# Performance work log

Hardware: AMD Instinct MI355X
Metric: run time of the kernel (lower is better)

## Reference

```python
import jax, jax.numpy as jnp
import numpy as np
import math
from jax import lax

B, L = 64, 8192
S = L // 8          # width after 3 stride-(1,2) SAME convs
D = 4 * 5           # height(4) * channels(5) -> per-token feature dim
D_FLAT = S * D


def setup_inputs():
    key = jax.random.key(0)
    ks = jax.random.split(key, 32)
    sc = 0.1
    inp = {
        "inputs": jax.random.randint(ks[0], (B, L), 0, 4, dtype=jnp.int32),
        # conv stack: HWIO kernels, Conv2D(5,(4,4),(1,2),'SAME')
        "conv_w1": sc * jax.random.normal(ks[1], (4, 4, 1, 5), jnp.float32),
        "conv_b1": jnp.zeros((5,), jnp.float32),
        "conv_w2": sc * jax.random.normal(ks[2], (4, 4, 5, 5), jnp.float32),
        "conv_b2": jnp.zeros((5,), jnp.float32),
        "conv_w3": sc * jax.random.normal(ks[3], (4, 4, 5, 5), jnp.float32),
        "conv_b3": jnp.zeros((5,), jnp.float32),
        # 3 SelfAttn blocks, each with K/Q/V projections [D, D]
        "attn1_K": sc * jax.random.normal(ks[4], (D, D), jnp.float32),
        "attn1_Q": sc * jax.random.normal(ks[5], (D, D), jnp.float32),
        "attn1_V": sc * jax.random.normal(ks[6], (D, D), jnp.float32),
        "attn2_K": sc * jax.random.normal(ks[7], (D, D), jnp.float32),
        "attn2_Q": sc * jax.random.normal(ks[8], (D, D), jnp.float32),
        "attn2_V": sc * jax.random.normal(ks[9], (D, D), jnp.float32),
        "attn3_K": sc * jax.random.normal(ks[10], (D, D), jnp.float32),
        "attn3_Q": sc * jax.random.normal(ks[11], (D, D), jnp.float32),
        "attn3_V": sc * jax.random.normal(ks[12], (D, D), jnp.float32),
        # 3 Dense(10) layers (no activation, as in Keras defaults)
        "dense_w1": 0.01 * jax.random.normal(ks[13], (D_FLAT, 10), jnp.float32),
        "dense_b1": jnp.zeros((10,), jnp.float32),
        "dense_w2": sc * jax.random.normal(ks[14], (10, 10), jnp.float32),
        "dense_b2": jnp.zeros((10,), jnp.float32),
        "dense_w3": sc * jax.random.normal(ks[15], (10, 10), jnp.float32),
        "dense_b3": jnp.zeros((10,), jnp.float32),
    }
    return inp


def _conv(x, w, b):
    # NHWC, HWIO, strides (1,2), SAME
    y = lax.conv_general_dilated(x, w, window_strides=(1, 2), padding="SAME",
                                 dimension_numbers=("NHWC", "HWIO", "NHWC"))
    return y + b


def _self_attn(x, Kw, Qw, Vw):
    # x: [B, S, D]; manual causal scaled dot-product attention
    K = x @ Kw
    Q = x @ Qw
    V = x @ Vw
    s = Q.shape[1]
    mask = jnp.triu(jnp.full((s, s), -jnp.inf, dtype=x.dtype), k=1)
    scores = jnp.einsum("bsd,btd->bst", Q, K) / math.sqrt(K.shape[-1]) + mask
    return jax.nn.softmax(scores, axis=-1) @ V


def reference(inputs, conv_w1, conv_b1, conv_w2, conv_b2, conv_w3, conv_b3,
              attn1_K, attn1_Q, attn1_V, attn2_K, attn2_Q, attn2_V,
              attn3_K, attn3_Q, attn3_V,
              dense_w1, dense_b1, dense_w2, dense_b2, dense_w3, dense_b3):
    # one_hot over axis=1 -> [B, 4, L], then channel dim -> [B, 4, L, 1]
    x = jax.nn.one_hot(inputs, 4, axis=1, dtype=jnp.float32)[..., None]
    x = _conv(x, conv_w1, conv_b1)
    x = _conv(x, conv_w2, conv_b2)
    x = _conv(x, conv_w3, conv_b3)            # [B, 4, S, 5]
    # tokens along width, features = height(4) x channels(5)
    x = jnp.transpose(x, (0, 2, 1, 3)).reshape(x.shape[0], S, D)
    x = _self_attn(x, attn1_K, attn1_Q, attn1_V)
    x = _self_attn(x, attn2_K, attn2_Q, attn2_V)
    x = _self_attn(x, attn3_K, attn3_Q, attn3_V)
    x = x.reshape(x.shape[0], -1)             # flatten [B, S*D]
    x = x @ dense_w1 + dense_b1
    x = x @ dense_w2 + dense_b2
    x = x @ dense_w3 + dense_b3               # [B, 10]
    return x
```

## Files before the change

### kernel.cpp

```cpp
#include <hip/hip_runtime.h>
#include <hip/hip_bf16.h>


#define B_ 64
#define L_ 8192
#define S_ 1024
#define D_ 20

typedef unsigned short ushort_t;
typedef __attribute__((ext_vector_type(8))) short short8_t;
typedef __attribute__((ext_vector_type(4))) short short4_t;
typedef __attribute__((ext_vector_type(4))) float f32x4_t;

__device__ __forceinline__ ushort_t f2bf(float f) {
  unsigned u = __float_as_uint(f);
  return (ushort_t)((u + 0x7fffu + ((u >> 16) & 1u)) >> 16);
}
__device__ __forceinline__ float bf2f(ushort_t h) {
  return __uint_as_float(((unsigned)h) << 16);
}

__global__ __launch_bounds__(256) void conv12_kernel(
    const int* __restrict__ inp,
    const float* __restrict__ W1c, const float* __restrict__ B1c,
    const float* __restrict__ W2c, const float* __restrict__ B2c,
    float* __restrict__ out,
    const float* __restrict__ W1d,
    float* __restrict__ W1T) {
  __shared__ float w1s[80], b1s[5], w2s[400], b2s[5];
  for (int j = threadIdx.x; j < 400; j += 256) w2s[j] = W2c[j];
  if (threadIdx.x < 80)      w1s[threadIdx.x]      = W1c[threadIdx.x];
  else if (threadIdx.x < 85) b1s[threadIdx.x - 80] = B1c[threadIdx.x - 80];
  else if (threadIdx.x < 90) b2s[threadIdx.x - 85] = B2c[threadIdx.x - 85];
  __syncthreads();
  const int idx = blockIdx.x * 256 + threadIdx.x;
  const int b  = idx >> 11;
  const int wo = idx & 2047;
  const int* ib = inp + (size_t)b * L_;
  int iv[10];
#pragma unroll
  for (int t = 0; t < 10; ++t) {
    int g = 4 * wo - 3 + t;
    iv[t] = (g >= 0 && g < L_) ? ib[g] : -100;
  }
  float val[4][4][5];
#pragma unroll
  for (int pos = 0; pos < 4; ++pos) {
    const int w1 = 2 * wo - 1 + pos;
    const bool okp = (w1 >= 0 && w1 < 4096);
#pragma unroll
    for (int hi = 0; hi < 4; ++hi)
#pragma unroll
      for (int ci = 0; ci < 5; ++ci) val[hi][pos][ci] = okp ? b1s[ci] : 0.f;
    if (okp) {
#pragma unroll
      for (int kw = 0; kw < 4; ++kw) {
        const int gw = 2 * w1 - 1 + kw;
        if (gw >= 0 && gw < L_) {
          const int v = iv[2 * pos + kw];
#pragma unroll
          for (int hi = 0; hi < 4; ++hi) {
            const int kh = v - hi + 1;
            if (kh >= 0 && kh < 4) {
#pragma unroll
              for (int ci = 0; ci < 5; ++ci)
                val[hi][pos][ci] += w1s[(kh * 4 + kw) * 5 + ci];
            }
          }
        }
      }
    }
  }
  float acc[4][5];
#pragma unroll
  for (int h = 0; h < 4; ++h)
#pragma unroll
    for (int c = 0; c < 5; ++c) acc[h][c] = b2s[c];
#pragma unroll
  for (int kh = 0; kh < 4; ++kh)
#pragma unroll
    for (int kw = 0; kw < 4; ++kw)
#pragma unroll
      for (int ci = 0; ci < 5; ++ci) {
        const float* wp = w2s + ((kh * 4 + kw) * 5 + ci) * 5;
        float w0 = wp[0], w1v = wp[1], w2v = wp[2], w3 = wp[3], w4 = wp[4];
#pragma unroll
        for (int h = 0; h < 4; ++h) {
          int hi = h - 1 + kh;
          if (hi >= 0 && hi < 4) {
            float x = val[hi][kw][ci];
            acc[h][0] += w0 * x;  acc[h][1] += w1v * x; acc[h][2] += w2v * x;
            acc[h][3] += w3 * x;  acc[h][4] += w4 * x;
          }
        }
      }
  float* ob = out + (size_t)b * 4 * 2048 * 5;
#pragma unroll
  for (int h = 0; h < 4; ++h)
#pragma unroll
    for (int c = 0; c < 5; ++c) ob[(h * 2048 + wo) * 5 + c] = acc[h][c];
  for (int j = idx; j < 204800; j += 131072) {
    int col = j / 20480, i2 = j - col * 20480;
    W1T[j] = W1d[i2 * 10 + col];
  }
}

__global__ __launch_bounds__(256) void conv3_proj_kernel(
    const float* __restrict__ in,
    const float* __restrict__ W,  const float* __restrict__ Bi,
    const float* __restrict__ Kw, const float* __restrict__ Qw,
    const float* __restrict__ Vw,
    ushort_t* __restrict__ Qb, ushort_t* __restrict__ Kb,
    ushort_t* __restrict__ Vt) {
  constexpr int WIN = 2048;
  __shared__ float ws[400], bs[5];
  __shared__ float kw[400], qw[400], vw[400];
  for (int j = threadIdx.x; j < 400; j += 256) {
    ws[j] = W[j]; kw[j] = Kw[j]; qw[j] = Qw[j]; vw[j] = Vw[j];
  }
  if (threadIdx.x < 5) bs[threadIdx.x] = Bi[threadIdx.x];
  __syncthreads();
  const int r  = blockIdx.x * 256 + threadIdx.x;
  const int b  = r >> 10;
  const int wo = r & 1023;
  float val[4][4][5];
#pragma unroll
  for (int hi = 0; hi < 4; ++hi) {
    const float* ir = in + ((size_t)b * 4 + hi) * WIN * 5;
#pragma unroll
    for (int kwp = 0; kwp < 4; ++kwp) {
      int wi = 2 * wo - 1 + kwp;
      bool ok = (wi >= 0 && wi < WIN);
#pragma unroll
      for (int ci = 0; ci < 5; ++ci) val[hi][kwp][ci] = ok ? ir[wi * 5 + ci] : 0.f;
    }
  }
  float acc[4][5];
#pragma unroll
  for (int h = 0; h < 4; ++h)
#pragma unroll
    for (int c = 0; c < 5; ++c) acc[h][c] = bs[c];
#pragma unroll
  for (int kh = 0; kh < 4; ++kh)
#pragma unroll
    for (int kwp = 0; kwp < 4; ++kwp)
#pragma unroll
      for (int ci = 0; ci < 5; ++ci) {
        const float* wp = ws + ((kh * 4 + kwp) * 5 + ci) * 5;
        float w0 = wp[0], w1 = wp[1], w2 = wp[2], w3 = wp[3], w4 = wp[4];
#pragma unroll
        for (int h = 0; h < 4; ++h) {
          int hi = h - 1 + kh;
          if (hi >= 0 && hi < 4) {
            float x = val[hi][kwp][ci];
            acc[h][0] += w0 * x; acc[h][1] += w1 * x; acc[h][2] += w2 * x;
            acc[h][3] += w3 * x; acc[h][4] += w4 * x;
          }
        }
      }
  float x[D_];
#pragma unroll
  for (int h = 0; h < 4; ++h)
#pragma unroll
    for (int c = 0; c < 5; ++c) x[h * 5 + c] = acc[h][c];
  float q[D_], k[D_], v[D_];
#pragma unroll
  for (int j = 0; j < D_; ++j) { q[j] = 0.f; k[j] = 0.f; v[j] = 0.f; }
#pragma unroll
  for (int i = 0; i < D_; ++i) {
#pragma unroll
    for (int j = 0; j < D_; ++j) {
      q[j] += x[i] * qw[i * D_ + j];
      k[j] += x[i] * kw[i * D_ + j];
      v[j] += x[i] * vw[i * D_ + j];
    }
  }
  const float sc = 0.22360679774997896f;
  ushort_t qt[32], kt[32];
#pragma unroll
  for (int j = 0; j < D_; ++j) { qt[j] = f2bf(q[j] * sc); kt[j] = f2bf(k[j]); }
#pragma unroll
  for (int j = D_; j < 32; ++j) { qt[j] = 0; kt[j] = 0; }
  int4* qd = (int4*)(Qb + (size_t)r * 32);
  int4* kd = (int4*)(Kb + (size_t)r * 32);
#pragma unroll
  for (int j = 0; j < 4; ++j) {
    qd[j] = *(const int4*)(qt + 8 * j);
    kd[j] = *(const int4*)(kt + 8 * j);
  }
  ushort_t* vbase = Vt + ((size_t)b * 32) * 1024 + wo;
#pragma unroll
  for (int d = 0; d < D_; ++d) vbase[d * 1024] = f2bf(v[d]);
}

#define TT_ 128
template <bool FUSE>
__global__ __launch_bounds__(256) void attn_kernel(
    const ushort_t* __restrict__ Qb, const ushort_t* __restrict__ Kb,
    const ushort_t* __restrict__ Vt,
    const float* __restrict__ Kw2, const float* __restrict__ Qw2,
    const float* __restrict__ Vw2,
    ushort_t* __restrict__ Qb2, ushort_t* __restrict__ Kb2,
    ushort_t* __restrict__ Vt2,
    const float* __restrict__ W1T,
    float* __restrict__ part2) {
  const int b     = blockIdx.y;
  const int g     = (blockIdx.y >> 4) & 3;
  const int off   = 4 * (g >> 1);
  const int strip = (g & 1) ? ((15 - off - blockIdx.x) & 15)
                            : (((int)blockIdx.x + off) & 15);
  const int q0    = strip * 64;
  const int tid   = threadIdx.x;
  const int w     = tid >> 6;
  const int lane  = tid & 63;
  const int n     = lane & 15;
  const int quad  = lane >> 4;
  const int qbase = q0 + 16 * w;
  const int qg    = qbase + n;
  __shared__ ushort_t kts[128 * 40];
  __shared__ ushort_t vts[32 * 136];
  __shared__ float extraf[FUSE ? 2480 : 3840];
  if (FUSE) {
    float tmp[5];
#pragma unroll
    for (int u = 0; u < 5; ++u) {
      int j = tid + u * 256;
      if (j < 1200) {
        int m = j / 400, oo = j - m * 400;
        tmp[u] = (m == 0) ? Kw2[oo] : (m == 1) ? Qw2[oo] : Vw2[oo];
      }
    }
#pragma unroll
    for (int u = 0; u < 5; ++u) {
      int j = tid + u * 256;
      if (j < 1200) extraf[j] = tmp[u];
    }
  }
  const ushort_t* KbB = Kb + (size_t)b * 1024 * 32;
  const ushort_t* VtB = Vt + (size_t)b * 32 * 1024;
  short8_t qfrag = *(const short8_t*)(Qb + ((size_t)(b * 1024 + qbase + n)) * 32 + quad * 8);
  f32x4_t oA = {0.f, 0.f, 0.f, 0.f};
  f32x4_t oB = {0.f, 0.f, 0.f, 0.f};
  float lsum = 0.f;
  const f32x4_t zero = {0.f, 0.f, 0.f, 0.f};
  const int nt = q0 + 64;
  for (int t0 = 0; t0 < nt; t0 += TT_) {
    __syncthreads();
    for (int i = tid; i < 512; i += 256) {
      int row = i >> 2, qc = i & 3;
      *(int4*)(kts + row * 40 + qc * 8) =
          *(const int4*)(KbB + (size_t)(t0 + row) * 32 + qc * 8);
    }
    for (int i = tid; i < 320; i += 256) {
      int row = i >> 4, cc = i & 15;
      *(int4*)(vts + row * 136 + cc * 8) =
          *(const int4*)(VtB + (size_t)row * 1024 + t0 + cc * 8);
    }
    __syncthreads();
    short8_t kf[8];
#pragma unroll
    for (int hc = 0; hc < 8; ++hc)
      kf[hc] = *(const short8_t*)(kts + (hc * 16 + n) * 40 + quad * 8);
#pragma unroll
    for (int hc = 0; hc < 8; ++hc) {
      const int tg = t0 + hc * 16 + quad * 4;
      f32x4_t s = __builtin_amdgcn_mfma_f32_16x16x32_bf16(kf[hc], qfrag, zero, 0, 0, 0);
      ushort_t pk4[4];
#pragma unroll
      for (int r = 0; r < 4; ++r) {
        float p = (tg + r <= qg) ? __expf(s[r]) : 0.f;
        ushort_t h = f2bf(p);
        lsum += bf2f(h);
        pk4[r] = h;
      }
      short4_t pfrag = *(const short4_t*)pk4;
      short4_t vlo = *(const short4_t*)(vts + n * 136 + hc * 16 + quad * 4);
      short4_t vhi = *(const short4_t*)(vts + (16 + n) * 136 + hc * 16 + quad * 4);
      oA = __builtin_amdgcn_mfma_f32_16x16x16bf16_1k(vlo, pfrag, oA, 0, 0, 0);
      oB = __builtin_amdgcn_mfma_f32_16x16x16bf16_1k(vhi, pfrag, oB, 0, 0, 0);
    }
  }
  float l = lsum;
  l += __shfl_xor(l, 16, 64);
  l += __shfl_xor(l, 32, 64);
  const float inv = 1.f / l;
  if (FUSE) {
    float* pw  = extraf;
    float* oxw = extraf + 1200 + w * 320;
#pragma unroll
    for (int r = 0; r < 4; ++r) oxw[n * 20 + quad * 4 + r] = oA[r] * inv;
    if (quad == 0) {
#pragma unroll
      for (int r = 0; r < 4; ++r) oxw[n * 20 + 16 + r] = oB[r] * inv;
    }
    __asm__ volatile("s_waitcnt lgkmcnt(0)" ::: "memory");
    const int row  = lane >> 2;
    const int part = lane & 3;
    float x[D_];
#pragma unroll
    for (int i = 0; i < D_; ++i) x[i] = oxw[row * 20 + i];
    float qv[5], kv[5], vv[5];
#pragma unroll
    for (int jj = 0; jj < 5; ++jj) { qv[jj] = 0.f; kv[jj] = 0.f; vv[jj] = 0.f; }
#pragma unroll
    for (int i = 0; i < D_; ++i) {
      const float xi = x[i];
#pragma unroll
      for (int jj = 0; jj < 5; ++jj) {
        const int j = 5 * part + jj;
        kv[jj] += xi * pw[i * 20 + j];
        qv[jj] += xi * pw[400 + i * 20 + j];
        vv[jj] += xi * pw[800 + i * 20 + j];
      }
    }
    const float sc = 0.22360679774997896f;
    const int rg = b * 1024 + qbase + row;
    const int s  = rg & 1023;
#pragma unroll
    for (int jj = 0; jj < 5; ++jj) {
      const int j = 5 * part + jj;
      Kb2[(size_t)rg * 32 + j] = f2bf(kv[jj]);
      Qb2[(size_t)rg * 32 + j] = f2bf(qv[jj] * sc);
      Vt2[(size_t)b * 32768 + (size_t)j * 1024 + s] = f2bf(vv[jj]);
    }
    if (part == 0) {
#pragma unroll
      for (int u = 0; u < 6; ++u)
        *(unsigned*)(Kb2 + (size_t)rg * 32 + 20 + 2 * u) = 0u;
    } else if (part == 1) {
#pragma unroll
      for (int u = 0; u < 6; ++u)
        *(unsigned*)(Qb2 + (size_t)rg * 32 + 20 + 2 * u) = 0u;
    }
  } else {
    float* oxflat = extraf;
    float* oxw    = oxflat + w * 320;
    float* red    = extraf + 1280;
#pragma unroll
    for (int r = 0; r < 4; ++r) oxw[n * 20 + quad * 4 + r] = oA[r] * inv;
    if (quad == 0) {
#pragma unroll
      for (int r = 0; r < 4; ++r) oxw[n * 20 + 16 + r] = oB[r] * inv;
    }
    __syncthreads();
    float acc[10];
#pragma unroll
    for (int j = 0; j < 10; ++j) acc[j] = 0.f;
    const float* wb = W1T;
    const int base = q0 * 20;
#pragma unroll
    for (int k = 0; k < 5; ++k) {
      const int il = tid + 256 * k;
      const float xv = oxflat[il];
#pragma unroll
      for (int j = 0; j < 10; ++j)
        acc[j] += xv * wb[(size_t)j * 20480 + base + il];
    }
#pragma unroll
    for (int j = 0; j < 10; ++j) red[tid * 10 + j] = acc[j];
    __syncthreads();
    for (int off2 = 128; off2 > 0; off2 >>= 1) {
      if (tid < off2) {
#pragma unroll
        for (int j = 0; j < 10; ++j) red[tid * 10 + j] += red[(tid + off2) * 10 + j];
      }
      __syncthreads();
    }
    if (tid < 10) part2[((b << 4) + strip) * 10 + tid] = red[tid];
  }
}

__global__ __launch_bounds__(64) void dense_final(
    const float* __restrict__ part2,
    const float* __restrict__ B1,
    const float* __restrict__ W2, const float* __restrict__ B2,
    const float* __restrict__ W3, const float* __restrict__ B3,
    float* __restrict__ out) {
  const int b = blockIdx.x;
  __shared__ float y1[10], y2[10];
  if (threadIdx.x < 10) {
    int j = threadIdx.x;
    float s = 0.f;
#pragma unroll
    for (int st = 0; st < 16; ++st) s += part2[((b << 4) + st) * 10 + j];
    y1[j] = s + B1[j];
  }
  __syncthreads();
  if (threadIdx.x < 10) {
    int j = threadIdx.x;
    float s = B2[j];
#pragma unroll
    for (int i = 0; i < 10; ++i) s += y1[i] * W2[i * 10 + j];
    y2[j] = s;
  }
  __syncthreads();
  if (threadIdx.x < 10) {
    int j = threadIdx.x;
    float s = B3[j];
#pragma unroll
    for (int i = 0; i < 10; ++i) s += y2[i] * W3[i * 10 + j];
    out[b * 10 + j] = s;
  }
}

extern "C" void kernel_launch(void* const* d_in, const int* in_sizes, int n_in,
                              void* d_out, int out_size, void* d_ws, size_t ws_size,
                              hipStream_t stream) {
  const int*   inp = (const int*)d_in[0];
  const float* cw1 = (const float*)d_in[1];
  const float* cb1 = (const float*)d_in[2];
  const float* cw2 = (const float*)d_in[3];
  const float* cb2 = (const float*)d_in[4];
  const float* cw3 = (const float*)d_in[5];
  const float* cb3 = (const float*)d_in[6];
  const float* a1K = (const float*)d_in[7];
  const float* a1Q = (const float*)d_in[8];
  const float* a1V = (const float*)d_in[9];
  const float* a2K = (const float*)d_in[10];
  const float* a2Q = (const float*)d_in[11];
  const float* a2V = (const float*)d_in[12];
  const float* a3K = (const float*)d_in[13];
  const float* a3Q = (const float*)d_in[14];
  const float* a3V = (const float*)d_in[15];
  const float* dw1 = (const float*)d_in[16];
  const float* db1 = (const float*)d_in[17];
  const float* dw2 = (const float*)d_in[18];
  const float* db2 = (const float*)d_in[19];
  const float* dw3 = (const float*)d_in[20];
  const float* db3 = (const float*)d_in[21];
  float* outp = (float*)d_out;

  float* wsf = (float*)d_ws;
  ushort_t* qbA  = (ushort_t*)(wsf);
  ushort_t* kbA  = (ushort_t*)(wsf + 1048576);
  ushort_t* vtA  = (ushort_t*)(wsf + 2097152);
  float*    part2= wsf + 4456448;
  float*    w1t  = wsf + 4466688;
  ushort_t* qbB  = (ushort_t*)(wsf + 4671488);
  ushort_t* kbB  = (ushort_t*)(wsf + 5712384);
  ushort_t* vtB  = (ushort_t*)(wsf + 6760960);
  float*    c2   = wsf + 5242880;

  conv12_kernel<<<512, 256, 0, stream>>>(inp, cw1, cb1, cw2, cb2, c2, dw1, w1t);

  conv3_proj_kernel<<<256, 256, 0, stream>>>(c2, cw3, cb3, a1K, a1Q, a1V, qbA, kbA, vtA);
  attn_kernel<true><<<dim3(16, 64), 256, 0, stream>>>(
      qbA, kbA, vtA, a2K, a2Q, a2V, qbB, kbB, vtB, nullptr, nullptr);
  attn_kernel<true><<<dim3(16, 64), 256, 0, stream>>>(
      qbB, kbB, vtB, a3K, a3Q, a3V, qbA, kbA, vtA, nullptr, nullptr);
  attn_kernel<false><<<dim3(16, 64), 256, 0, stream>>>(
      qbA, kbA, vtA, nullptr, nullptr, nullptr, nullptr, nullptr, nullptr,
      w1t, part2);

  dense_final<<<64, 64, 0, stream>>>(part2, db1, dw2, db2, dw3, db3, outp);
}
```

Baseline: 216.2 us.

## Load K/V fragments directly from global memory, dropping LDS staging in attention

The attention loop no longer stages 128-key K and V tiles in shared memory behind two barriers per iteration. Each wave now reads its MFMA fragments straight from global memory in 64-key steps and relies on L1/L2 for reuse across waves. This removes the per-tile syncthreads and LDS traffic, frees shared memory for occupancy, and drops wasted keys past the causal limit. The cost is redundant global loads by each of the four waves and less coalesced strided V reads. A barrier is added before the fused epilogue so extraf is written before it is read.

```diff
diff --git a/kernel.cpp b/kernel.cpp
--- a/kernel.cpp
+++ b/kernel.cpp
@@ -193,7 +193,6 @@
   for (int d = 0; d < D_; ++d) vbase[d * 1024] = f2bf(v[d]);
 }
 
-#define TT_ 128
 template <bool FUSE>
 __global__ __launch_bounds__(256) void attn_kernel(
     const ushort_t* __restrict__ Qb, const ushort_t* __restrict__ Kb,
@@ -217,8 +216,6 @@
   const int quad  = lane >> 4;
   const int qbase = q0 + 16 * w;
   const int qg    = qbase + n;
-  __shared__ ushort_t kts[128 * 40];
-  __shared__ ushort_t vts[32 * 136];
   __shared__ float extraf[FUSE ? 2480 : 3840];
   if (FUSE) {
     float tmp[5];
@@ -243,28 +240,21 @@
   f32x4_t oB = {0.f, 0.f, 0.f, 0.f};
   float lsum = 0.f;
   const f32x4_t zero = {0.f, 0.f, 0.f, 0.f};
-  const int nt = q0 + 64;
-  for (int t0 = 0; t0 < nt; t0 += TT_) {
-    __syncthreads();
-    for (int i = tid; i < 512; i += 256) {
-      int row = i >> 2, qc = i & 3;
-      *(int4*)(kts + row * 40 + qc * 8) =
-          *(const int4*)(KbB + (size_t)(t0 + row) * 32 + qc * 8);
-    }
-    for (int i = tid; i < 320; i += 256) {
-      int row = i >> 4, cc = i & 15;
-      *(int4*)(vts + row * 136 + cc * 8) =
-          *(const int4*)(VtB + (size_t)row * 1024 + t0 + cc * 8);
-    }
-    __syncthreads();
-    short8_t kf[8];
-#pragma unroll
-    for (int hc = 0; hc < 8; ++hc)
-      kf[hc] = *(const short8_t*)(kts + (hc * 16 + n) * 40 + quad * 8);
-#pragma unroll
-    for (int hc = 0; hc < 8; ++hc) {
-      const int tg = t0 + hc * 16 + quad * 4;
-      f32x4_t s = __builtin_amdgcn_mfma_f32_16x16x32_bf16(kf[hc], qfrag, zero, 0, 0, 0);
+  const int niter = strip + 1;
+  for (int it = 0; it < niter; ++it) {
+    const int t0 = it * 64;
+    short8_t kf[4];
+    short4_t vl[4], vh[4];
+#pragma unroll
+    for (int j = 0; j < 4; ++j) {
+      kf[j] = *(const short8_t*)(KbB + (size_t)(t0 + j * 16 + n) * 32 + quad * 8);
+      vl[j] = *(const short4_t*)(VtB + (size_t)n * 1024 + t0 + j * 16 + quad * 4);
+      vh[j] = *(const short4_t*)(VtB + (size_t)(16 + n) * 1024 + t0 + j * 16 + quad * 4);
+    }
+#pragma unroll
+    for (int j = 0; j < 4; ++j) {
+      const int tg = t0 + j * 16 + quad * 4;
+      f32x4_t s = __builtin_amdgcn_mfma_f32_16x16x32_bf16(kf[j], qfrag, zero, 0, 0, 0);
       ushort_t pk4[4];
 #pragma unroll
       for (int r = 0; r < 4; ++r) {
@@ -274,10 +264,8 @@
         pk4[r] = h;
       }
       short4_t pfrag = *(const short4_t*)pk4;
-      short4_t vlo = *(const short4_t*)(vts + n * 136 + hc * 16 + quad * 4);
-      short4_t vhi = *(const short4_t*)(vts + (16 + n) * 136 + hc * 16 + quad * 4);
-      oA = __builtin_amdgcn_mfma_f32_16x16x16bf16_1k(vlo, pfrag, oA, 0, 0, 0);
-      oB = __builtin_amdgcn_mfma_f32_16x16x16bf16_1k(vhi, pfrag, oB, 0, 0, 0);
+      oA = __builtin_amdgcn_mfma_f32_16x16x16bf16_1k(vl[j], pfrag, oA, 0, 0, 0);
+      oB = __builtin_amdgcn_mfma_f32_16x16x16bf16_1k(vh[j], pfrag, oB, 0, 0, 0);
     }
   }
   float l = lsum;
@@ -285,6 +273,7 @@
   l += __shfl_xor(l, 32, 64);
   const float inv = 1.f / l;
   if (FUSE) {
+    __syncthreads();
     float* pw  = extraf;
     float* oxw = extraf + 1200 + w * 320;
 #pragma unroll
```

After: 267.0 us. 23.5% more time.

## Split causal attention across key tiles with separate combine-and-project kernels

Applied to the files above, without the earlier changes.

Each attention layer is split key-wise, flash-decoding style. Every block handles one 128-key tile for a 64-query strip, covering only the tiles on or below the causal diagonal, and writes unnormalized partial outputs and row sums to a workspace. A combine kernel then sums the partials, normalizes, and applies the next layer's projection or the first dense layer. This evens out the causal load imbalance and greatly raises the block count, at the cost of extra kernel launches and a large fp32 partial buffer written to and read back from global memory.

```diff
diff --git a/kernel.cpp b/kernel.cpp
--- a/kernel.cpp
+++ b/kernel.cpp
@@ -193,181 +193,177 @@
   for (int d = 0; d < D_; ++d) vbase[d * 1024] = f2bf(v[d]);
 }
 
-#define TT_ 128
-template <bool FUSE>
-__global__ __launch_bounds__(256) void attn_kernel(
+__global__ __launch_bounds__(256) void attn_core(
     const ushort_t* __restrict__ Qb, const ushort_t* __restrict__ Kb,
     const ushort_t* __restrict__ Vt,
-    const float* __restrict__ Kw2, const float* __restrict__ Qw2,
-    const float* __restrict__ Vw2,
-    ushort_t* __restrict__ Qb2, ushort_t* __restrict__ Kb2,
-    ushort_t* __restrict__ Vt2,
-    const float* __restrict__ W1T,
-    float* __restrict__ part2) {
-  const int b     = blockIdx.y;
-  const int g     = (blockIdx.y >> 4) & 3;
-  const int off   = 4 * (g >> 1);
-  const int strip = (g & 1) ? ((15 - off - blockIdx.x) & 15)
-                            : (((int)blockIdx.x + off) & 15);
-  const int q0    = strip * 64;
-  const int tid   = threadIdx.x;
-  const int w     = tid >> 6;
-  const int lane  = tid & 63;
-  const int n     = lane & 15;
-  const int quad  = lane >> 4;
-  const int qbase = q0 + 16 * w;
-  const int qg    = qbase + n;
-  __shared__ ushort_t kts[128 * 40];
+    float* __restrict__ Opart,
+    float* __restrict__ lpart) {
+  const int id = blockIdx.x;
+  const int b  = id & 63;
+  int j = id >> 6;
+  int tg = 0;
+  while (j >= 16 - 2 * tg) { j -= 16 - 2 * tg; ++tg; }
+  const int sub  = j;
+  const int tid  = threadIdx.x;
+  const int w    = tid >> 6;
+  const int lane = tid & 63;
+  const int n    = lane & 15;
+  const int quad = lane >> 4;
+  const int qb   = 8 * tg + sub * 4 + w;
+  const int t0   = tg * 128;
   __shared__ ushort_t vts[32 * 136];
-  __shared__ float extraf[FUSE ? 2480 : 3840];
-  if (FUSE) {
-    float tmp[5];
-#pragma unroll
-    for (int u = 0; u < 5; ++u) {
-      int j = tid + u * 256;
-      if (j < 1200) {
-        int m = j / 400, oo = j - m * 400;
-        tmp[u] = (m == 0) ? Kw2[oo] : (m == 1) ? Qw2[oo] : Vw2[oo];
-      }
-    }
-#pragma unroll
-    for (int u = 0; u < 5; ++u) {
-      int j = tid + u * 256;
-      if (j < 1200) extraf[j] = tmp[u];
-    }
+  const ushort_t* VtB = Vt + (size_t)b * 32 * 1024;
+  for (int i = tid; i < 320; i += 256) {
+    int row = i >> 4, cc = i & 15;
+    *(int4*)(vts + row * 136 + cc * 8) =
+        *(const int4*)(VtB + (size_t)row * 1024 + t0 + cc * 8);
   }
   const ushort_t* KbB = Kb + (size_t)b * 1024 * 32;
-  const ushort_t* VtB = Vt + (size_t)b * 32 * 1024;
-  short8_t qfrag = *(const short8_t*)(Qb + ((size_t)(b * 1024 + qbase + n)) * 32 + quad * 8);
+  const int qg = qb * 16 + n;
+  short8_t qfrag = *(const short8_t*)(Qb + ((size_t)(b * 1024 + qb * 16 + n)) * 32 + quad * 8);
+  short8_t kf[8];
+#pragma unroll
+  for (int c = 0; c < 8; ++c)
+    kf[c] = *(const short8_t*)(KbB + (size_t)(t0 + c * 16 + n) * 32 + quad * 8);
   f32x4_t oA = {0.f, 0.f, 0.f, 0.f};
   f32x4_t oB = {0.f, 0.f, 0.f, 0.f};
+  const f32x4_t zero = {0.f, 0.f, 0.f, 0.f};
   float lsum = 0.f;
-  const f32x4_t zero = {0.f, 0.f, 0.f, 0.f};
-  const int nt = q0 + 64;
-  for (int t0 = 0; t0 < nt; t0 += TT_) {
-    __syncthreads();
-    for (int i = tid; i < 512; i += 256) {
-      int row = i >> 2, qc = i & 3;
-      *(int4*)(kts + row * 40 + qc * 8) =
-          *(const int4*)(KbB + (size_t)(t0 + row) * 32 + qc * 8);
-    }
-    for (int i = tid; i < 320; i += 256) {
-      int row = i >> 4, cc = i & 15;
-      *(int4*)(vts + row * 136 + cc * 8) =
-          *(const int4*)(VtB + (size_t)row * 1024 + t0 + cc * 8);
-    }
-    __syncthreads();
-    short8_t kf[8];
-#pragma unroll
-    for (int hc = 0; hc < 8; ++hc)
-      kf[hc] = *(const short8_t*)(kts + (hc * 16 + n) * 40 + quad * 8);
-#pragma unroll
-    for (int hc = 0; hc < 8; ++hc) {
-      const int tg = t0 + hc * 16 + quad * 4;
-      f32x4_t s = __builtin_amdgcn_mfma_f32_16x16x32_bf16(kf[hc], qfrag, zero, 0, 0, 0);
-      ushort_t pk4[4];
-#pragma unroll
-      for (int r = 0; r < 4; ++r) {
-        float p = (tg + r <= qg) ? __expf(s[r]) : 0.f;
-        ushort_t h = f2bf(p);
-        lsum += bf2f(h);
-        pk4[r] = h;
-      }
-      short4_t pfrag = *(const short4_t*)pk4;
-      short4_t vlo = *(const short4_t*)(vts + n * 136 + hc * 16 + quad * 4);
-      short4_t vhi = *(const short4_t*)(vts + (16 + n) * 136 + hc * 16 + quad * 4);
-      oA = __builtin_amdgcn_mfma_f32_16x16x16bf16_1k(vlo, pfrag, oA, 0, 0, 0);
-      oB = __builtin_amdgcn_mfma_f32_16x16x16bf16_1k(vhi, pfrag, oB, 0, 0, 0);
-    }
+  __syncthreads();
+#pragma unroll
+  for (int c = 0; c < 8; ++c) {
+    const int tgl = t0 + c * 16 + quad * 4;
+    f32x4_t s = __builtin_amdgcn_mfma_f32_16x16x32_bf16(kf[c], qfrag, zero, 0, 0, 0);
+    ushort_t pk4[4];
+#pragma unroll
+    for (int r = 0; r < 4; ++r) {
+      float p = (tgl + r <= qg) ? __expf(s[r]) : 0.f;
+      ushort_t h = f2bf(p);
+      lsum += bf2f(h);
+      pk4[r] = h;
+    }
+    short4_t pfrag = *(const short4_t*)pk4;
+    short4_t vlo = *(const short4_t*)(vts + n * 136 + c * 16 + quad * 4);
+    short4_t vhi = *(const short4_t*)(vts + (16 + n) * 136 + c * 16 + quad * 4);
+    oA = __builtin_amdgcn_mfma_f32_16x16x16bf16_1k(vlo, pfrag, oA, 0, 0, 0);
+    oB = __builtin_amdgcn_mfma_f32_16x16x16bf16_1k(vhi, pfrag, oB, 0, 0, 0);
   }
   float l = lsum;
   l += __shfl_xor(l, 16, 64);
   l += __shfl_xor(l, 32, 64);
+  float* Ob = Opart + (((size_t)tg * 64 + b) * 1024 + qb * 16 + n) * 20;
+  *(f32x4_t*)(Ob + quad * 4) = oA;
+  if (quad == 0) {
+    *(f32x4_t*)(Ob + 16) = oB;
+    lpart[((size_t)tg * 64 + b) * 1024 + qb * 16 + n] = l;
+  }
+}
+
+__global__ __launch_bounds__(256) void combine_proj(
+    const float* __restrict__ Opart, const float* __restrict__ lpart,
+    const float* __restrict__ Kw, const float* __restrict__ Qw,
+    const float* __restrict__ Vw,
+    ushort_t* __restrict__ Qb2, ushort_t* __restrict__ Kb2,
+    ushort_t* __restrict__ Vt2) {
+  __shared__ float kw[400], qw[400], vw[400];
+  for (int i = threadIdx.x; i < 400; i += 256) {
+    kw[i] = Kw[i]; qw[i] = Qw[i]; vw[i] = Vw[i];
+  }
+  __syncthreads();
+  const int r = blockIdx.x * 256 + threadIdx.x;
+  const int b = r >> 10, q = r & 1023;
+  const int nslots = (q >> 7) + 1;
+  float x[D_]; float l = 0.f;
+#pragma unroll
+  for (int i = 0; i < D_; ++i) x[i] = 0.f;
+  for (int s = 0; s < nslots; ++s) {
+    const float* Ob = Opart + (((size_t)s * 64 + b) * 1024 + q) * 20;
+#pragma unroll
+    for (int i = 0; i < D_; ++i) x[i] += Ob[i];
+    l += lpart[((size_t)s * 64 + b) * 1024 + q];
+  }
   const float inv = 1.f / l;
-  if (FUSE) {
-    float* pw  = extraf;
-    float* oxw = extraf + 1200 + w * 320;
-#pragma unroll
-    for (int r = 0; r < 4; ++r) oxw[n * 20 + quad * 4 + r] = oA[r] * inv;
-    if (quad == 0) {
-#pragma unroll
-      for (int r = 0; r < 4; ++r) oxw[n * 20 + 16 + r] = oB[r] * inv;
-    }
-    __asm__ volatile("s_waitcnt lgkmcnt(0)" ::: "memory");
-    const int row  = lane >> 2;
-    const int part = lane & 3;
-    float x[D_];
-#pragma unroll
-    for (int i = 0; i < D_; ++i) x[i] = oxw[row * 20 + i];
-    float qv[5], kv[5], vv[5];
-#pragma unroll
-    for (int jj = 0; jj < 5; ++jj) { qv[jj] = 0.f; kv[jj] = 0.f; vv[jj] = 0.f; }
-#pragma unroll
-    for (int i = 0; i < D_; ++i) {
-      const float xi = x[i];
-#pragma unroll
-      for (int jj = 0; jj < 5; ++jj) {
-        const int j = 5 * part + jj;
-        kv[jj] += xi * pw[i * 20 + j];
-        qv[jj] += xi * pw[400 + i * 20 + j];
-        vv[jj] += xi * pw[800 + i * 20 + j];
-      }
-    }
-    const float sc = 0.22360679774997896f;
-    const int rg = b * 1024 + qbase + row;
-    const int s  = rg & 1023;
-#pragma unroll
-    for (int jj = 0; jj < 5; ++jj) {
-      const int j = 5 * part + jj;
-      Kb2[(size_t)rg * 32 + j] = f2bf(kv[jj]);
-      Qb2[(size_t)rg * 32 + j] = f2bf(qv[jj] * sc);
-      Vt2[(size_t)b * 32768 + (size_t)j * 1024 + s] = f2bf(vv[jj]);
-    }
-    if (part == 0) {
-#pragma unroll
-      for (int u = 0; u < 6; ++u)
-        *(unsigned*)(Kb2 + (size_t)rg * 32 + 20 + 2 * u) = 0u;
-    } else if (part == 1) {
-#pragma unroll
-      for (int u = 0; u < 6; ++u)
-        *(unsigned*)(Qb2 + (size_t)rg * 32 + 20 + 2 * u) = 0u;
-    }
-  } else {
-    float* oxflat = extraf;
-    float* oxw    = oxflat + w * 320;
-    float* red    = extraf + 1280;
-#pragma unroll
-    for (int r = 0; r < 4; ++r) oxw[n * 20 + quad * 4 + r] = oA[r] * inv;
-    if (quad == 0) {
-#pragma unroll
-      for (int r = 0; r < 4; ++r) oxw[n * 20 + 16 + r] = oB[r] * inv;
+#pragma unroll
+  for (int i = 0; i < D_; ++i) x[i] *= inv;
+  float qv[D_], kv[D_], vv[D_];
+#pragma unroll
+  for (int j = 0; j < D_; ++j) { qv[j] = 0.f; kv[j] = 0.f; vv[j] = 0.f; }
+#pragma unroll
+  for (int i = 0; i < D_; ++i) {
+#pragma unroll
+    for (int j = 0; j < D_; ++j) {
+      qv[j] += x[i] * qw[i * D_ + j];
+      kv[j] += x[i] * kw[i * D_ + j];
+      vv[j] += x[i] * vw[i * D_ + j];
+    }
+  }
+  const float sc = 0.22360679774997896f;
+  ushort_t qt[32], kt[32];
+#pragma unroll
+  for (int j = 0; j < D_; ++j) { qt[j] = f2bf(qv[j] * sc); kt[j] = f2bf(kv[j]); }
+#pragma unroll
+  for (int j = D_; j < 32; ++j) { qt[j] = 0; kt[j] = 0; }
+  int4* qd = (int4*)(Qb2 + (size_t)r * 32);
+  int4* kd = (int4*)(Kb2 + (size_t)r * 32);
+#pragma unroll
+  for (int j = 0; j < 4; ++j) {
+    qd[j] = *(const int4*)(qt + 8 * j);
+    kd[j] = *(const int4*)(kt + 8 * j);
+  }
+  ushort_t* vbase = Vt2 + ((size_t)b * 32) * 1024 + q;
+#pragma unroll
+  for (int d = 0; d < D_; ++d) vbase[d * 1024] = f2bf(vv[d]);
+}
+
+__global__ __launch_bounds__(256) void combine_dense(
+    const float* __restrict__ Opart, const float* __restrict__ lpart,
+    const float* __restrict__ W1T,
+    float* __restrict__ part2) {
+  const int b   = blockIdx.y;
+  const int bx  = blockIdx.x;
+  const int tid = threadIdx.x;
+  __shared__ float oxflat[1280];
+  __shared__ float red[2560];
+  const int rr   = tid >> 2;
+  const int part = tid & 3;
+  const int q    = bx * 64 + rr;
+  const int nslots = (q >> 7) + 1;
+  float xv[5]; float l = 0.f;
+#pragma unroll
+  for (int t = 0; t < 5; ++t) xv[t] = 0.f;
+  for (int s = 0; s < nslots; ++s) {
+    const float* Ob = Opart + (((size_t)s * 64 + b) * 1024 + q) * 20 + 5 * part;
+#pragma unroll
+    for (int t = 0; t < 5; ++t) xv[t] += Ob[t];
+    l += lpart[((size_t)s * 64 + b) * 1024 + q];
+  }
+  const float inv = 1.f / l;
+#pragma unroll
+  for (int t = 0; t < 5; ++t) oxflat[rr * 20 + 5 * part + t] = xv[t] * inv;
+  __syncthreads();
+  float acc[10];
+#pragma unroll
+  for (int o = 0; o < 10; ++o) acc[o] = 0.f;
+  const int base = bx * 1280;
+#pragma unroll
+  for (int k = 0; k < 5; ++k) {
+    const int il = tid + 256 * k;
+    const float v = oxflat[il];
+#pragma unroll
+    for (int o = 0; o < 10; ++o)
+      acc[o] += v * W1T[(size_t)o * 20480 + base + il];
+  }
+#pragma unroll
+  for (int o = 0; o < 10; ++o) red[tid * 10 + o] = acc[o];
+  __syncthreads();
+  for (int off2 = 128; off2 > 0; off2 >>= 1) {
+    if (tid < off2) {
+#pragma unroll
+      for (int o = 0; o < 10; ++o) red[tid * 10 + o] += red[(tid + off2) * 10 + o];
     }
     __syncthreads();
-    float acc[10];
-#pragma unroll
-    for (int j = 0; j < 10; ++j) acc[j] = 0.f;
-    const float* wb = W1T;
-    const int base = q0 * 20;
-#pragma unroll
-    for (int k = 0; k < 5; ++k) {
-      const int il = tid + 256 * k;
-      const float xv = oxflat[il];
-#pragma unroll
-      for (int j = 0; j < 10; ++j)
-        acc[j] += xv * wb[(size_t)j * 20480 + base + il];
-    }
-#pragma unroll
-    for (int j = 0; j < 10; ++j) red[tid * 10 + j] = acc[j];
-    __syncthreads();
-    for (int off2 = 128; off2 > 0; off2 >>= 1) {
-      if (tid < off2) {
-#pragma unroll
-        for (int j = 0; j < 10; ++j) red[tid * 10 + j] += red[(tid + off2) * 10 + j];
-      }
-      __syncthreads();
-    }
-    if (tid < 10) part2[((b << 4) + strip) * 10 + tid] = red[tid];
-  }
+  }
+  if (tid < 10) part2[((b << 4) + bx) * 10 + tid] = red[tid];
 }
 
 __global__ __launch_bounds__(64) void dense_final(
@@ -440,17 +436,19 @@
   ushort_t* kbB  = (ushort_t*)(wsf + 5712384);
   ushort_t* vtB  = (ushort_t*)(wsf + 6760960);
   float*    c2   = wsf + 5242880;
+  float*    opart= wsf + 7864320;
+  float*    lpart= wsf + 18350080;
 
   conv12_kernel<<<512, 256, 0, stream>>>(inp, cw1, cb1, cw2, cb2, c2, dw1, w1t);
 
   conv3_proj_kernel<<<256, 256, 0, stream>>>(c2, cw3, cb3, a1K, a1Q, a1V, qbA, kbA, vtA);
-  attn_kernel<true><<<dim3(16, 64), 256, 0, stream>>>(
-      qbA, kbA, vtA, a2K, a2Q, a2V, qbB, kbB, vtB, nullptr, nullptr);
-  attn_kernel<true><<<dim3(16, 64), 256, 0, stream>>>(
-      qbB, kbB, vtB, a3K, a3Q, a3V, qbA, kbA, vtA, nullptr, nullptr);
-  attn_kernel<false><<<dim3(16, 64), 256, 0, stream>>>(
-      qbA, kbA, vtA, nullptr, nullptr, nullptr, nullptr, nullptr, nullptr,
-      w1t, part2);
+
+  attn_core<<<4608, 256, 0, stream>>>(qbA, kbA, vtA, opart, lpart);
+  combine_proj<<<256, 256, 0, stream>>>(opart, lpart, a2K, a2Q, a2V, qbB, kbB, vtB);
+  attn_core<<<4608, 256, 0, stream>>>(qbB, kbB, vtB, opart, lpart);
+  combine_proj<<<256, 256, 0, stream>>>(opart, lpart, a3K, a3Q, a3V, qbA, kbA, vtA);
+  attn_core<<<4608, 256, 0, stream>>>(qbA, kbA, vtA, opart, lpart);
+  combine_dense<<<dim3(16, 64), 256, 0, stream>>>(opart, lpart, w1t, part2);
 
   dense_final<<<64, 64, 0, stream>>>(part2, db1, dw2, db2, dw3, db3, outp);
 }
```

New measurement: 228.0 us. 1.05x slower.
